# Kernel optimization log

Measured on AMD Instinct MI355X. Metric: run time of the kernel, lower is better.

The kernel has to match this reference:

```python
import jax, jax.numpy as jnp
import numpy as np


def setup_inputs() -> dict:
    key = jax.random.key(0)
    kx, kw = jax.random.split(key)
    x = jax.random.normal(kx, (32, 256, 56, 56), dtype=jnp.float32)
    # kaiming-uniform-like init for weights [O, I, K, K]
    fan_in = 256 * 3 * 3
    bound = float(np.sqrt(6.0 / fan_in))
    weights = jax.random.uniform(kw, (256, 256, 3, 3), dtype=jnp.float32,
                                 minval=-bound, maxval=bound)
    return {"x": x, "weights": weights}


def reference(x, weights):
    # Binarize weights with sign (STE is a backward-only concern; forward uses sign).
    qw = jnp.sign(weights)
    # conv2d, NCHW / OIHW, stride 1, no padding, no bias
    out = jax.lax.conv_general_dilated(
        x, qw,
        window_strides=(1, 1),
        padding="VALID",
        dimension_numbers=("NCHW", "OIHW", "NCHW"),
    )
    return out
```

## Files before the change

### kernel.cpp

```cpp
#include <hip/hip_runtime.h>
#include <cstdint>

#define NB 32
#define IC 256
#define OC 256
#define H 56
#define WIDTH 56
#define OH 54
#define OW 54
#define HW (H*WIDTH)
#define OHW (OH*OW)
#define KTOT 2304
#define M_TOT (NB*OHW)
#define C8N (IC/8)

#define BM 128
#define BO 256
#define BK 32
#define KSTEPS (KTOT/BK)
#define MBLOCKS (M_TOT/BM)

__device__ __align__(16) unsigned short g_qwt[KSTEPS*BO*BK];
__device__ __align__(16) unsigned short g_xq[NB*C8N*HW*8];

typedef __bf16 bf16x8 __attribute__((ext_vector_type(8)));
typedef float  f32x4  __attribute__((ext_vector_type(4)));

typedef __attribute__((address_space(1))) const unsigned int gas_u32;
typedef __attribute__((address_space(3))) unsigned int las_u32;
__device__ __forceinline__ void async_copy16(const void* g, void* l) {
  __builtin_amdgcn_global_load_lds((gas_u32*)g, (las_u32*)l, 16, 0, 0);
}

__device__ inline unsigned short f32_bf16(float f) {
  union { float f; unsigned int u; } v; v.f = f;
  unsigned int u = v.u;
  return (unsigned short)((u + 0x7FFFu + ((u >> 16) & 1u)) >> 16);
}

#define WAITV(N) asm volatile("s_waitcnt vmcnt(" #N ")" ::: "memory")
#define BARRIER() do { \
  __builtin_amdgcn_sched_barrier(0); \
  __builtin_amdgcn_s_barrier(); \
  __builtin_amdgcn_sched_barrier(0); \
} while (0)

__global__ __launch_bounds__(256) void repack_w(const float* __restrict__ w) {
  int L = blockIdx.x * 256 + threadIdx.x;
  int step = L >> 13;
  int r    = (L >> 5) & 255;
  int kc   = L & 31;
  int cs   = kc >> 3;
  int b    = kc & 7;
  int csrc = cs ^ ((r >> 1) & 3);
  int k    = step*BK + csrc*8 + b;
  int pos  = k >> 8;
  int c    = k & 255;
  float v = w[r*2304 + c*9 + pos];
  unsigned short s = (v > 0.f) ? 0x3F80u : ((v < 0.f) ? 0xBF80u : 0u);
  g_qwt[L] = s;
}

__global__ __launch_bounds__(256) void xform_x(const float* __restrict__ x) {
  int g = blockIdx.x * 256 + threadIdx.x;
  int hw = g % HW;
  int tc = g / HW;
  int c8 = tc & 31;
  int n  = tc >> 5;
  const float* src = x + (n*IC + c8*8)*HW + hw;
  unsigned int o[4];
  #pragma unroll
  for (int j = 0; j < 4; ++j) {
    unsigned int lo = f32_bf16(src[(2*j+0)*HW]);
    unsigned int hi = f32_bf16(src[(2*j+1)*HW]);
    o[j] = lo | (hi << 16);
  }
  *(uint4*)(&g_xq[g*8]) = *(uint4*)o;
}

__global__ __launch_bounds__(512, 4) void bconv_gemm(float* __restrict__ out) {
  __shared__ __align__(16) unsigned short Wl[3][BO*BK];
  __shared__ __align__(16) unsigned short Xl[3][BM*BK];
  const int t = threadIdx.x;

  const int orig = blockIdx.x;
  const int xcd  = orig & 7;
  const int idx  = orig >> 3;
  const int bm   = (xcd == 0) ? idx : (92 + (xcd - 1)*91 + idx);
  const int m0   = bm * BM;

  int xbase;
  {
    const int i   = t >> 2;
    const int cs  = t & 3;
    const int csw = cs ^ ((i >> 1) & 3);
    int m  = m0 + i;
    int n  = m / OHW;
    int rm = m - n*OHW;
    int oh = rm / OW;
    int ow = rm - oh*OW;
    xbase = ((n*C8N + csw)*HW + oh*WIDTH + ow) * 8;
  }

  const int lane = t & 63;
  const int wv   = t >> 6;
  const int col  = lane & 15;
  const int quad = lane >> 4;
  const int wo   = (wv >> 1) * 64;
  const int wm   = (wv & 1) * 64;
  const int sw   = (quad ^ ((col >> 1) & 3)) * 8;
  int aoff[4], boff[4];
  #pragma unroll
  for (int i = 0; i < 4; ++i) {
    aoff[i] = (wo + i*16 + col)*BK + sw;
    boff[i] = (wm + i*16 + col)*BK + sw;
  }

  auto STAGE = [&](int step, int buf) {
    const unsigned short* ws = g_qwt + step*(BO*BK);
    async_copy16(&ws[t*8],       &Wl[buf][t*8]);
    async_copy16(&ws[(t+512)*8], &Wl[buf][(t+512)*8]);
    const int pos = step >> 3;
    const int kh  = pos / 3;
    const int kw  = pos - kh*3;
    const int xo  = xbase + (((step & 7)*4)*HW + kh*WIDTH + kw)*8;
    async_copy16(&g_xq[xo], &Xl[buf][t*8]);
  };

  f32x4 acc[4][4];
  #pragma unroll
  for (int a = 0; a < 4; ++a)
    #pragma unroll
    for (int b = 0; b < 4; ++b)
      acc[a][b] = (f32x4){0.f, 0.f, 0.f, 0.f};

  auto COMPUTE = [&](const unsigned short* Wb, const unsigned short* Xb) {
    bf16x8 av[4], bv[4];
    #pragma unroll
    for (int i = 0; i < 4; ++i) av[i] = *(const bf16x8*)(&Wb[aoff[i]]);
    #pragma unroll
    for (int i = 0; i < 4; ++i) bv[i] = *(const bf16x8*)(&Xb[boff[i]]);
    __builtin_amdgcn_s_setprio(1);
    #pragma unroll
    for (int io = 0; io < 4; ++io)
      #pragma unroll
      for (int im = 0; im < 4; ++im)
        acc[io][im] = __builtin_amdgcn_mfma_f32_16x16x32_bf16(av[io], bv[im], acc[io][im], 0, 0, 0);
    __builtin_amdgcn_s_setprio(0);
  };

  STAGE(0, 0);
  STAGE(1, 1);
  STAGE(2, 2);
  WAITV(6);
  BARRIER();
  COMPUTE(Wl[0], Xl[0]);

  #pragma unroll 1
  for (int s = 1; s < 68; s += 3) {
    BARRIER();
    STAGE(s + 2, 0);
    WAITV(6);
    BARRIER();
    COMPUTE(Wl[1], Xl[1]);

    BARRIER();
    STAGE(s + 3, 1);
    WAITV(6);
    BARRIER();
    COMPUTE(Wl[2], Xl[2]);

    BARRIER();
    STAGE(s + 4, 2);
    WAITV(6);
    BARRIER();
    COMPUTE(Wl[0], Xl[0]);
  }

  BARRIER();
  WAITV(3);
  BARRIER();
  COMPUTE(Wl[1], Xl[1]);
  BARRIER();
  WAITV(0);
  BARRIER();
  COMPUTE(Wl[2], Xl[2]);

  #pragma unroll
  for (int im = 0; im < 4; ++im) {
    int m  = m0 + wm + im*16 + col;
    int n  = m / OHW;
    int rm = m - n*OHW;
    float* obase = out + n*(OC*OHW) + rm;
    #pragma unroll
    for (int io = 0; io < 4; ++io) {
      int orow = wo + io*16 + quad*4;
      #pragma unroll
      for (int r = 0; r < 4; ++r)
        obase[(orow + r)*OHW] = acc[io][im][r];
    }
  }
}

extern "C" void kernel_launch(void* const* d_in, const int* in_sizes, int n_in,
                              void* d_out, int out_size, void* d_ws, size_t ws_size,
                              hipStream_t stream) {
  const float* x = (const float*)d_in[0];
  const float* w = (const float*)d_in[1];
  float* out = (float*)d_out;

  repack_w<<<dim3((KSTEPS*BO*BK)/256), 256, 0, stream>>>(w);
  xform_x <<<dim3((NB*C8N*HW)/256), 256, 0, stream>>>(x);
  bconv_gemm<<<dim3(MBLOCKS), 512, 0, stream>>>(out);
}
```

Before: 312.3 us.

## Switch to 32x32x16 MFMA, restructure LDS pipeline, fuse prep kernels

Replaces the 16x16x32 bf16 MFMA tiles with 32x32x16 MFMAs (2x2 tiles of f32x16 accumulators per wave), which halves the LDS fragment loads per step and changes the output write pattern. The triple-buffered main loop now issues the next async stage before computing on the current buffer and uses one barrier per step instead of two, so loads overlap compute more. The weight-repack and input-transform kernels are merged into one launch to save a kernel launch. The larger MFMA shape changes register pressure and the layout of output stores.

After: 322.0 us. 3.1% more time.

```diff
diff --git a/kernel.cpp b/kernel.cpp
--- a/kernel.cpp
+++ b/kernel.cpp
@@ -19,12 +19,13 @@
 #define BK 32
 #define KSTEPS (KTOT/BK)
 #define MBLOCKS (M_TOT/BM)
+#define XBLK ((NB*C8N*HW)/256)
 
 __device__ __align__(16) unsigned short g_qwt[KSTEPS*BO*BK];
 __device__ __align__(16) unsigned short g_xq[NB*C8N*HW*8];
 
 typedef __bf16 bf16x8 __attribute__((ext_vector_type(8)));
-typedef float  f32x4  __attribute__((ext_vector_type(4)));
+typedef float  f32x16 __attribute__((ext_vector_type(16)));
 
 typedef __attribute__((address_space(1))) const unsigned int gas_u32;
 typedef __attribute__((address_space(3))) unsigned int las_u32;
@@ -45,37 +46,38 @@
   __builtin_amdgcn_sched_barrier(0); \
 } while (0)
 
-__global__ __launch_bounds__(256) void repack_w(const float* __restrict__ w) {
-  int L = blockIdx.x * 256 + threadIdx.x;
-  int step = L >> 13;
-  int r    = (L >> 5) & 255;
-  int kc   = L & 31;
-  int cs   = kc >> 3;
-  int b    = kc & 7;
-  int csrc = cs ^ ((r >> 1) & 3);
-  int k    = step*BK + csrc*8 + b;
-  int pos  = k >> 8;
-  int c    = k & 255;
-  float v = w[r*2304 + c*9 + pos];
-  unsigned short s = (v > 0.f) ? 0x3F80u : ((v < 0.f) ? 0xBF80u : 0u);
-  g_qwt[L] = s;
-}
-
-__global__ __launch_bounds__(256) void xform_x(const float* __restrict__ x) {
-  int g = blockIdx.x * 256 + threadIdx.x;
-  int hw = g % HW;
-  int tc = g / HW;
-  int c8 = tc & 31;
-  int n  = tc >> 5;
-  const float* src = x + (n*IC + c8*8)*HW + hw;
-  unsigned int o[4];
-  #pragma unroll
-  for (int j = 0; j < 4; ++j) {
-    unsigned int lo = f32_bf16(src[(2*j+0)*HW]);
-    unsigned int hi = f32_bf16(src[(2*j+1)*HW]);
-    o[j] = lo | (hi << 16);
-  }
-  *(uint4*)(&g_xq[g*8]) = *(uint4*)o;
+__global__ __launch_bounds__(256) void prep(const float* __restrict__ x,
+                                            const float* __restrict__ w) {
+  const int t = threadIdx.x;
+  if (blockIdx.x < XBLK) {
+    int g = blockIdx.x * 256 + t;
+    int hw = g % HW;
+    int tc = g / HW;
+    int c8 = tc & 31;
+    int n  = tc >> 5;
+    const float* src = x + (n*IC + c8*8)*HW + hw;
+    unsigned int o[4];
+    #pragma unroll
+    for (int j = 0; j < 4; ++j) {
+      unsigned int lo = f32_bf16(src[(2*j+0)*HW]);
+      unsigned int hi = f32_bf16(src[(2*j+1)*HW]);
+      o[j] = lo | (hi << 16);
+    }
+    *(uint4*)(&g_xq[g*8]) = *(uint4*)o;
+  } else {
+    int L = (blockIdx.x - XBLK) * 256 + t;
+    int step = L >> 13;
+    int r    = (L >> 5) & 255;
+    int kc   = L & 31;
+    int cs   = kc >> 3;
+    int b    = kc & 7;
+    int csrc = cs ^ ((r >> 1) & 3);
+    int k    = step*BK + csrc*8 + b;
+    int pos  = k >> 8;
+    int c    = k & 255;
+    float v = w[r*2304 + c*9 + pos];
+    g_qwt[L] = (v > 0.f) ? 0x3F80u : ((v < 0.f) ? 0xBF80u : 0u);
+  }
 }
 
 __global__ __launch_bounds__(512, 4) void bconv_gemm(float* __restrict__ out) {
@@ -104,17 +106,17 @@
 
   const int lane = t & 63;
   const int wv   = t >> 6;
-  const int col  = lane & 15;
-  const int quad = lane >> 4;
+  const int r5   = lane & 31;
+  const int half = lane >> 5;
   const int wo   = (wv >> 1) * 64;
   const int wm   = (wv & 1) * 64;
-  const int sw   = (quad ^ ((col >> 1) & 3)) * 8;
-  int aoff[4], boff[4];
+  const int swz  = (r5 >> 1) & 3;
+  int koff[2];
   #pragma unroll
-  for (int i = 0; i < 4; ++i) {
-    aoff[i] = (wo + i*16 + col)*BK + sw;
-    boff[i] = (wm + i*16 + col)*BK + sw;
-  }
+  for (int kk = 0; kk < 2; ++kk)
+    koff[kk] = (((kk << 1) | half) ^ swz) * 8;
+  const int aRow = (wo + r5) * BK;
+  const int bRow = (wm + r5) * BK;
 
   auto STAGE = [&](int step, int buf) {
     const unsigned short* ws = g_qwt + step*(BO*BK);
@@ -127,77 +129,82 @@
     async_copy16(&g_xq[xo], &Xl[buf][t*8]);
   };
 
-  f32x4 acc[4][4];
+  f32x16 acc[2][2];
   #pragma unroll
-  for (int a = 0; a < 4; ++a)
-    #pragma unroll
-    for (int b = 0; b < 4; ++b)
-      acc[a][b] = (f32x4){0.f, 0.f, 0.f, 0.f};
+  for (int a = 0; a < 2; ++a)
+    #pragma unroll
+    for (int b = 0; b < 2; ++b)
+      acc[a][b] = (f32x16)0.f;
 
   auto COMPUTE = [&](const unsigned short* Wb, const unsigned short* Xb) {
-    bf16x8 av[4], bv[4];
-    #pragma unroll
-    for (int i = 0; i < 4; ++i) av[i] = *(const bf16x8*)(&Wb[aoff[i]]);
-    #pragma unroll
-    for (int i = 0; i < 4; ++i) bv[i] = *(const bf16x8*)(&Xb[boff[i]]);
+    bf16x8 av[2][2], bv[2][2];
+    #pragma unroll
+    for (int kk = 0; kk < 2; ++kk) {
+      #pragma unroll
+      for (int ot = 0; ot < 2; ++ot)
+        av[ot][kk] = *(const bf16x8*)(&Wb[aRow + ot*(32*BK) + koff[kk]]);
+      #pragma unroll
+      for (int mt = 0; mt < 2; ++mt)
+        bv[mt][kk] = *(const bf16x8*)(&Xb[bRow + mt*(32*BK) + koff[kk]]);
+    }
     __builtin_amdgcn_s_setprio(1);
     #pragma unroll
-    for (int io = 0; io < 4; ++io)
-      #pragma unroll
-      for (int im = 0; im < 4; ++im)
-        acc[io][im] = __builtin_amdgcn_mfma_f32_16x16x32_bf16(av[io], bv[im], acc[io][im], 0, 0, 0);
+    for (int kk = 0; kk < 2; ++kk)
+      #pragma unroll
+      for (int ot = 0; ot < 2; ++ot)
+        #pragma unroll
+        for (int mt = 0; mt < 2; ++mt)
+          acc[ot][mt] = __builtin_amdgcn_mfma_f32_32x32x16_bf16(
+              av[ot][kk], bv[mt][kk], acc[ot][mt], 0, 0, 0);
     __builtin_amdgcn_s_setprio(0);
   };
 
   STAGE(0, 0);
   STAGE(1, 1);
-  STAGE(2, 2);
-  WAITV(6);
+  WAITV(3);
   BARRIER();
+
+  #pragma unroll 1
+  for (int s = 0; s < 69; s += 3) {
+    STAGE(s + 2, 2); __builtin_amdgcn_sched_barrier(0);
+    COMPUTE(Wl[0], Xl[0]);
+    WAITV(3);
+    BARRIER();
+
+    STAGE(s + 3, 0); __builtin_amdgcn_sched_barrier(0);
+    COMPUTE(Wl[1], Xl[1]);
+    WAITV(3);
+    BARRIER();
+
+    STAGE(s + 4, 1); __builtin_amdgcn_sched_barrier(0);
+    COMPUTE(Wl[2], Xl[2]);
+    WAITV(3);
+    BARRIER();
+  }
+
+  STAGE(71, 2); __builtin_amdgcn_sched_barrier(0);
   COMPUTE(Wl[0], Xl[0]);
-
-  #pragma unroll 1
-  for (int s = 1; s < 68; s += 3) {
-    BARRIER();
-    STAGE(s + 2, 0);
-    WAITV(6);
-    BARRIER();
-    COMPUTE(Wl[1], Xl[1]);
-
-    BARRIER();
-    STAGE(s + 3, 1);
-    WAITV(6);
-    BARRIER();
-    COMPUTE(Wl[2], Xl[2]);
-
-    BARRIER();
-    STAGE(s + 4, 2);
-    WAITV(6);
-    BARRIER();
-    COMPUTE(Wl[0], Xl[0]);
-  }
-
-  BARRIER();
   WAITV(3);
   BARRIER();
   COMPUTE(Wl[1], Xl[1]);
-  BARRIER();
   WAITV(0);
   BARRIER();
   COMPUTE(Wl[2], Xl[2]);
 
   #pragma unroll
-  for (int im = 0; im < 4; ++im) {
-    int m  = m0 + wm + im*16 + col;
+  for (int mt = 0; mt < 2; ++mt) {
+    int m  = m0 + wm + mt*32 + r5;
     int n  = m / OHW;
     int rm = m - n*OHW;
     float* obase = out + n*(OC*OHW) + rm;
     #pragma unroll
-    for (int io = 0; io < 4; ++io) {
-      int orow = wo + io*16 + quad*4;
-      #pragma unroll
-      for (int r = 0; r < 4; ++r)
-        obase[(orow + r)*OHW] = acc[io][im][r];
+    for (int ot = 0; ot < 2; ++ot) {
+      int o0 = wo + ot*32 + half*4;
+      #pragma unroll
+      for (int reg = 0; reg < 16; ++reg) {
+        int o = o0 + (reg & 3) + 8*(reg >> 2);
+        obase[o*OHW] = acc[ot][mt][reg];
+      }
     }
   }
 }
@@ -209,7 +216,6 @@
   const float* w = (const float*)d_in[1];
   float* out = (float*)d_out;
 
-  repack_w<<<dim3((KSTEPS*BO*BK)/256), 256, 0, stream>>>(w);
-  xform_x <<<dim3((NB*C8N*HW)/256), 256, 0, stream>>>(x);
+  prep<<<dim3(XBLK + (KSTEPS*BO*BK)/256), 256, 0, stream>>>(x, w);
   bconv_gemm<<<dim3(MBLOCKS), 512, 0, stream>>>(out);
 }
```

## Restructure GEMM pipeline to one barrier per step and fuse prep kernels

Applied to the files above, without the earlier changes.

Rewrites the triple-buffered main loop so each step issues the next async copy and then computes on the current buffer, with a single wait and barrier per step instead of two. This cuts synchronization overhead and lets copies overlap MFMA work, at the cost of one fewer stage prefetched ahead. Also merges the weight repack and input bf16 conversion into one prep launch to remove one kernel launch.

Result: no change. 309.9 us (-0.8%).

```diff
diff --git a/kernel.cpp b/kernel.cpp
--- a/kernel.cpp
+++ b/kernel.cpp
@@ -19,6 +19,7 @@
 #define BK 32
 #define KSTEPS (KTOT/BK)
 #define MBLOCKS (M_TOT/BM)
+#define XBLK ((NB*C8N*HW)/256)
 
 __device__ __align__(16) unsigned short g_qwt[KSTEPS*BO*BK];
 __device__ __align__(16) unsigned short g_xq[NB*C8N*HW*8];
@@ -45,37 +46,38 @@
   __builtin_amdgcn_sched_barrier(0); \
 } while (0)
 
-__global__ __launch_bounds__(256) void repack_w(const float* __restrict__ w) {
-  int L = blockIdx.x * 256 + threadIdx.x;
-  int step = L >> 13;
-  int r    = (L >> 5) & 255;
-  int kc   = L & 31;
-  int cs   = kc >> 3;
-  int b    = kc & 7;
-  int csrc = cs ^ ((r >> 1) & 3);
-  int k    = step*BK + csrc*8 + b;
-  int pos  = k >> 8;
-  int c    = k & 255;
-  float v = w[r*2304 + c*9 + pos];
-  unsigned short s = (v > 0.f) ? 0x3F80u : ((v < 0.f) ? 0xBF80u : 0u);
-  g_qwt[L] = s;
-}
-
-__global__ __launch_bounds__(256) void xform_x(const float* __restrict__ x) {
-  int g = blockIdx.x * 256 + threadIdx.x;
-  int hw = g % HW;
-  int tc = g / HW;
-  int c8 = tc & 31;
-  int n  = tc >> 5;
-  const float* src = x + (n*IC + c8*8)*HW + hw;
-  unsigned int o[4];
-  #pragma unroll
-  for (int j = 0; j < 4; ++j) {
-    unsigned int lo = f32_bf16(src[(2*j+0)*HW]);
-    unsigned int hi = f32_bf16(src[(2*j+1)*HW]);
-    o[j] = lo | (hi << 16);
-  }
-  *(uint4*)(&g_xq[g*8]) = *(uint4*)o;
+__global__ __launch_bounds__(256) void prep(const float* __restrict__ x,
+                                            const float* __restrict__ w) {
+  const int t = threadIdx.x;
+  if (blockIdx.x < XBLK) {
+    int g = blockIdx.x * 256 + t;
+    int hw = g % HW;
+    int tc = g / HW;
+    int c8 = tc & 31;
+    int n  = tc >> 5;
+    const float* src = x + (n*IC + c8*8)*HW + hw;
+    unsigned int o[4];
+    #pragma unroll
+    for (int j = 0; j < 4; ++j) {
+      unsigned int lo = f32_bf16(src[(2*j+0)*HW]);
+      unsigned int hi = f32_bf16(src[(2*j+1)*HW]);
+      o[j] = lo | (hi << 16);
+    }
+    *(uint4*)(&g_xq[g*8]) = *(uint4*)o;
+  } else {
+    int L = (blockIdx.x - XBLK) * 256 + t;
+    int step = L >> 13;
+    int r    = (L >> 5) & 255;
+    int kc   = L & 31;
+    int cs   = kc >> 3;
+    int b    = kc & 7;
+    int csrc = cs ^ ((r >> 1) & 3);
+    int k    = step*BK + csrc*8 + b;
+    int pos  = k >> 8;
+    int c    = k & 255;
+    float v = w[r*2304 + c*9 + pos];
+    g_qwt[L] = (v > 0.f) ? 0x3F80u : ((v < 0.f) ? 0xBF80u : 0u);
+  }
 }
 
 __global__ __launch_bounds__(512, 4) void bconv_gemm(float* __restrict__ out) {
@@ -151,37 +153,32 @@
 
   STAGE(0, 0);
   STAGE(1, 1);
-  STAGE(2, 2);
-  WAITV(6);
+  WAITV(3);
   BARRIER();
+
+  #pragma unroll 1
+  for (int s = 0; s < 69; s += 3) {
+    STAGE(s + 2, 2); __builtin_amdgcn_sched_barrier(0);
+    COMPUTE(Wl[0], Xl[0]);
+    WAITV(3);
+    BARRIER();
+
+    STAGE(s + 3, 0); __builtin_amdgcn_sched_barrier(0);
+    COMPUTE(Wl[1], Xl[1]);
+    WAITV(3);
+    BARRIER();
+
+    STAGE(s + 4, 1); __builtin_amdgcn_sched_barrier(0);
+    COMPUTE(Wl[2], Xl[2]);
+    WAITV(3);
+    BARRIER();
+  }
+
+  STAGE(71, 2); __builtin_amdgcn_sched_barrier(0);
   COMPUTE(Wl[0], Xl[0]);
-
-  #pragma unroll 1
-  for (int s = 1; s < 68; s += 3) {
-    BARRIER();
-    STAGE(s + 2, 0);
-    WAITV(6);
-    BARRIER();
-    COMPUTE(Wl[1], Xl[1]);
-
-    BARRIER();
-    STAGE(s + 3, 1);
-    WAITV(6);
-    BARRIER();
-    COMPUTE(Wl[2], Xl[2]);
-
-    BARRIER();
-    STAGE(s + 4, 2);
-    WAITV(6);
-    BARRIER();
-    COMPUTE(Wl[0], Xl[0]);
-  }
-
-  BARRIER();
   WAITV(3);
   BARRIER();
   COMPUTE(Wl[1], Xl[1]);
-  BARRIER();
   WAITV(0);
   BARRIER();
   COMPUTE(Wl[2], Xl[2]);
@@ -209,7 +206,6 @@
   const float* w = (const float*)d_in[1];
   float* out = (float*)d_out;
 
-  repack_w<<<dim3((KSTEPS*BO*BK)/256), 256, 0, stream>>>(w);
-  xform_x <<<dim3((NB*C8N*HW)/256), 256, 0, stream>>>(x);
+  prep<<<dim3(XBLK + (KSTEPS*BO*BK)/256), 256, 0, stream>>>(x, w);
   bconv_gemm<<<dim3(MBLOCKS), 512, 0, stream>>>(out);
 }
```
